# Optimization experiments

Hardware: AMD Instinct MI355X
Metric: run time of the kernel (lower is better)

The kernel has to match this reference:

```python
import jax, jax.numpy as jnp
import numpy as np

DIM = 128
N_GNN = 3
VDW_N = 6.0
MAX_VDW = 0.0356
MIN_VDW = 0.0178
DEV_VDW_RADIUS = 0.2
DM_MIN = 0.5


def gated_gat(x, adj, W, Wb, A, gW, gb):
    # PIGNet-style GatedGAT: attention from bilinear form, gated residual
    h = x @ W + Wb                                   # [B,N,D]
    e = jnp.einsum('bjl,bkl->bjk', h @ A, h)
    e = e + jnp.swapaxes(e, 1, 2)
    att = jnp.where(adj > 0, e, -9e15)
    att = jax.nn.softmax(att, axis=-1) * adj
    hp = jax.nn.relu(jnp.einsum('bij,bjd->bid', att, h))
    coeff = jax.nn.sigmoid(jnp.concatenate([x, hp], axis=-1) @ gW + gb)  # [B,N,1]
    return coeff * x + (1.0 - coeff) * hp


def pair_mlp(lig, tgt, W1, b1, W2, b2):
    # MLP on concat([lig_i, tgt_j]) without materializing [B,L,T,2D]:
    # split W1 along its input dim (exact same math as concat @ W1)
    D = lig.shape[-1]
    pre = (jnp.einsum('bld,dk->blk', lig, W1[:D])[:, :, None, :]
           + jnp.einsum('btd,dk->btk', tgt, W1[D:])[:, None, :, :] + b1)
    h = jax.nn.relu(pre)                             # [B,L,T,D]
    return jnp.einsum('bltk,ko->blt', h, W2) + b2[0]  # [B,L,T]


def setup_inputs() -> dict:
    key = jax.random.key(0)
    ks = jax.random.split(key, 20)
    B, L, T, D = 8, 128, 512, DIM
    f32 = jnp.float32

    def adj(k, n, p):
        a = (jax.random.uniform(k, (B, n, n)) < p).astype(f32)
        a = jnp.maximum(a, jnp.swapaxes(a, 1, 2))
        return jnp.minimum(a + jnp.eye(n, dtype=f32), 1.0)

    s = 0.05
    inp = dict(
        ligand_h=jax.random.normal(ks[0], (B, L, 54), f32),
        target_h=jax.random.normal(ks[1], (B, T, 54), f32),
        ligand_adj=adj(ks[2], L, 0.10),
        target_adj=adj(ks[3], T, 0.02),
        interaction_indice=(jax.random.uniform(ks[4], (B, 3, L, T)) < 0.05).astype(f32),
        ligand_pos=jax.random.uniform(ks[5], (B, L, 3), f32) * 20.0,
        target_pos=jax.random.uniform(ks[6], (B, T, 3), f32) * 20.0,
        rotor=jnp.floor(jax.random.uniform(ks[7], (B, 1), f32) * 10.0),
        ligand_vdw_radii=jax.random.uniform(ks[8], (B, L), f32) * 0.5 + 1.5,
        target_vdw_radii=jax.random.uniform(ks[9], (B, T), f32) * 0.5 + 1.5,
        ligand_valid=jnp.ones((B, L), f32),
        target_valid=jnp.ones((B, T), f32),
        emb_W=jax.random.normal(ks[10], (54, D), f32) * s,
        gat_W=jax.random.normal(ks[11], (N_GNN, D, D), f32) * s,
        gat_Wb=jnp.zeros((N_GNN, D), f32),
        gat_A=jax.random.normal(ks[12], (N_GNN, D, D), f32) * s,
        gat_gW=jax.random.normal(ks[13], (N_GNN, 2 * D, 1), f32) * s,
        gat_gb=jnp.zeros((N_GNN, 1), f32),
        vdwA_W1=jax.random.normal(ks[14], (2 * D, D), f32) * s,
        vdwA_b1=jnp.zeros((D,), f32),
        vdwA_W2=jax.random.normal(ks[15], (D, 1), f32) * s,
        vdwA_b2=jnp.zeros((1,), f32),
        dc_W1=jax.random.normal(ks[16], (2 * D, D), f32) * s,
        dc_b1=jnp.zeros((D,), f32),
        dc_W2=jax.random.normal(ks[17], (D, 1), f32) * s,
        dc_b2=jnp.zeros((1,), f32),
        hbond_coeff=jnp.array([1.0], f32),
        metal_coeff=jnp.array([1.0], f32),
        hydrophobic_coeff=jnp.array([0.5], f32),
        rotor_coeff=jnp.array([0.5], f32),
    )
    return inp


def reference(ligand_h, target_h, ligand_adj, target_adj, interaction_indice,
              ligand_pos, target_pos, rotor, ligand_vdw_radii, target_vdw_radii,
              ligand_valid, target_valid, emb_W, gat_W, gat_Wb, gat_A, gat_gW,
              gat_gb, vdwA_W1, vdwA_b1, vdwA_W2, vdwA_b2, dc_W1, dc_b1, dc_W2,
              dc_b2, hbond_coeff, metal_coeff, hydrophobic_coeff, rotor_coeff):
    lig = ligand_h @ emb_W
    tgt = target_h @ emb_W
    # pairwise distance matrix with min-distance clamp
    diff = ligand_pos[:, :, None, :] - target_pos[:, None, :, :]
    dm = jnp.sqrt((diff * diff).sum(-1) + 1e-10)      # [B,L,T]
    dm = jnp.where(dm < DM_MIN, 1e10, dm)
    for i in range(N_GNN):  # eval mode: dropout is identity
        lig = gated_gat(lig, ligand_adj, gat_W[i], gat_Wb[i], gat_A[i], gat_gW[i], gat_gb[i])
        tgt = gated_gat(tgt, target_adj, gat_W[i], gat_Wb[i], gat_A[i], gat_gW[i], gat_gb[i])
    vdws_sum = ligand_vdw_radii[:, :, None] + target_vdw_radii[:, None, :]
    # dm_correction=True: tanh MLP on pairwise concat features, scaled by dev_vdw_radius
    vdws_sum = vdws_sum + jnp.tanh(pair_mlp(lig, tgt, dc_W1, dc_b1, dc_W2, dc_b2)) * DEV_VDW_RADIUS
    # --- vdw term ---
    dm_0 = jnp.where(vdws_sum < 1e-4, 1.0, vdws_sum)
    ratio = dm_0 / dm
    valid = ligand_valid[:, :, None] * target_valid[:, None, :]
    energy = jnp.minimum(ratio ** (2.0 * VDW_N) - 2.0 * ratio ** VDW_N, 100.0) * valid
    A = jax.nn.sigmoid(pair_mlp(lig, tgt, vdwA_W1, vdwA_b1, vdwA_W2, vdwA_b2))
    A = A * (MAX_VDW - MIN_VDW) + MIN_VDW
    vdw_e = (A * energy).sum((1, 2))                  # [B]
    # --- hbond / metal / hydrophobic ramps share dm - vdws_sum ---
    d = dm - vdws_sum
    ramp = jnp.clip(d / -0.7, 0.0, 1.0)
    hbond_e = -(hbond_coeff[0] ** 2) * (ramp * interaction_indice[:, 0]).sum((1, 2))
    metal_e = -(metal_coeff[0] ** 2) * (ramp * interaction_indice[:, 1]).sum((1, 2))
    ramp2 = jnp.clip(-d + 1.5, 0.0, 1.0)
    hydro_e = -(hydrophobic_coeff[0] ** 2) * (ramp2 * interaction_indice[:, 2]).sum((1, 2))
    energies = jnp.stack([vdw_e, hbond_e, metal_e, hydro_e], axis=-1)  # [B,4]
    energies = energies / (1.0 + rotor_coeff[0] ** 2 * rotor)          # rotor penalty
    return energies
```

## Files before the change

### kernel.cpp

```cpp
#include <hip/hip_runtime.h>
#include <hip/hip_bf16.h>
#include <math.h>

typedef __hip_bfloat16 bf16;

#define DIMD 128
#define BB 8
#define LL 128
#define TT 512

#define BMT 64
#define BKT 32
#define TGT_TILES 36
#define LIG_TILES 3

#define CV_EMBW   0L
#define CV_GATW   (CV_EMBW + 54 * 128)
#define CV_GATA   (CV_GATW + 3 * 128 * 128)
#define CV_WB     (CV_GATA + 3 * 128 * 128)
#define CV_GGW    (CV_WB + 3 * 128)
#define CV_GGB    (CV_GGW + 3 * 2 * 128)
#define CV_DCW1   (CV_GGB + 4)
#define CV_VW1    (CV_DCW1 + 2 * 128 * 128)
#define CV_TOTAL  (CV_VW1 + 2 * 128 * 128)

__device__ __forceinline__ float LD(const void* p, long i, int bf) {
    if (bf) return __bfloat162float(((const bf16*)p)[i]);
    return ((const float*)p)[i];
}

__global__ void init_cvt(const unsigned int* __restrict__ embw_raw,
                         const void* __restrict__ embW, const void* __restrict__ gatW,
                         const void* __restrict__ gatA, const void* __restrict__ gatWb,
                         const void* __restrict__ ggW, const void* __restrict__ ggb,
                         const void* __restrict__ dcW1, const void* __restrict__ vW1,
                         float* __restrict__ out, float* __restrict__ accum,
                         int* __restrict__ flagp) {
    __shared__ int cnts;
    int t = threadIdx.x;
    if (t == 0) cnts = 0;
    __syncthreads();
    unsigned int bword = (embw_raw[t] >> 8) & 0xffu;
    unsigned int e = bword & 0x7fu;
    if (e >= 0x38u && e <= 0x3fu) atomicAdd(&cnts, 1);
    __syncthreads();
    int bf = cnts > 128;
    if (blockIdx.x == 0) {
        if (t < 32) accum[t] = 0.0f;
        if (t == 0) *flagp = bf;
    }
    long i = (long)blockIdx.x * 256 + t;
    if (i >= CV_TOTAL) return;
    float v;
    if (i < CV_GATW)      v = LD(embW, i, bf);
    else if (i < CV_GATA) v = LD(gatW, i - CV_GATW, bf);
    else if (i < CV_WB)   v = LD(gatA, i - CV_GATA, bf);
    else if (i < CV_GGW)  v = LD(gatWb, i - CV_WB, bf);
    else if (i < CV_GGB)  v = LD(ggW, i - CV_GGW, bf);
    else if (i < CV_DCW1) { long j = i - CV_GGB; v = (j < 3) ? LD(ggb, j, bf) : 0.0f; }
    else if (i < CV_VW1)  v = LD(dcW1, i - CV_DCW1, bf);
    else                  v = LD(vW1, i - CV_VW1, bf);
    out[i] = v;
}

__global__ void embed_both(const void* __restrict__ Xl, const void* __restrict__ Xt,
                           const float* __restrict__ Wf, float* __restrict__ out,
                           int K, const int* __restrict__ flagp) {
    __shared__ float xrow[DIMD];
    int bf = *flagp;
    int row = blockIdx.x;
    int d = threadIdx.x;
    const void* X; long r;
    if (row < BB * LL) { X = Xl; r = row; }
    else               { X = Xt; r = row - BB * LL; }
    if (d < K) xrow[d] = LD(X, r * K + d, bf);
    __syncthreads();
    float acc = 0.0f;
    for (int k = 0; k < K; ++k)
        acc = fmaf(xrow[k], Wf[(long)k * DIMD + d], acc);
    out[(long)row * DIMD + d] = acc;
}

__global__ void gemm_hha_gate(float* __restrict__ X, const float* __restrict__ P0,
                              const float* __restrict__ P1, const float* __restrict__ P2,
                              const float* __restrict__ P3, const float* __restrict__ cvw,
                              int layer, int dogate,
                              float* __restrict__ hout, float* __restrict__ hAout) {
    __shared__ float xs[4][DIMD];
    __shared__ float hs[4][DIMD];
    __shared__ float gred[4][2];
    long row0 = (long)blockIdx.x * 4;
    int d = threadIdx.x & 127, rg = threadIdx.x >> 7;
    int w = threadIdx.x >> 6, lane = threadIdx.x & 63;
    long r0 = row0 + rg * 2, r1 = r0 + 1;
    float xv0 = X[r0 * DIMD + d];
    float xv1 = X[r1 * DIMD + d];
    if (dogate) {
        const float* gW = cvw + CV_GGW + (long)(layer - 1) * 2 * DIMD;
        float gb = cvw[CV_GGB + (layer - 1)];
        float hp0 = fmaxf(P0[r0 * DIMD + d] + P1[r0 * DIMD + d]
                        + P2[r0 * DIMD + d] + P3[r0 * DIMD + d], 0.0f);
        float hp1 = fmaxf(P0[r1 * DIMD + d] + P1[r1 * DIMD + d]
                        + P2[r1 * DIMD + d] + P3[r1 * DIMD + d], 0.0f);
        float s0 = xv0 * gW[d] + hp0 * gW[DIMD + d];
        float s1 = xv1 * gW[d] + hp1 * gW[DIMD + d];
#pragma unroll
        for (int s = 32; s > 0; s >>= 1) { s0 += __shfl_xor(s0, s); s1 += __shfl_xor(s1, s); }
        if (lane == 0) { gred[rg * 2 + 0][w & 1] = s0; gred[rg * 2 + 1][w & 1] = s1; }
        __syncthreads();
        float g0 = gred[rg * 2 + 0][0] + gred[rg * 2 + 0][1] + gb;
        float g1 = gred[rg * 2 + 1][0] + gred[rg * 2 + 1][1] + gb;
        float c0 = 1.0f / (1.0f + expf(-g0));
        float c1 = 1.0f / (1.0f + expf(-g1));
        xv0 = c0 * xv0 + (1.0f - c0) * hp0;
        xv1 = c1 * xv1 + (1.0f - c1) * hp1;
        X[r0 * DIMD + d] = xv0;
        X[r1 * DIMD + d] = xv1;
    }
    xs[rg * 2 + 0][d] = xv0;
    xs[rg * 2 + 1][d] = xv1;
    __syncthreads();
    const float* W = cvw + CV_GATW + (long)layer * DIMD * DIMD;
    const float* A = cvw + CV_GATA + (long)layer * DIMD * DIMD;
    float b = cvw[CV_WB + layer * DIMD + d];
    float h0 = b, h1 = b;
    const float* x0 = xs[rg * 2];
    const float* x1 = xs[rg * 2 + 1];
#pragma unroll 8
    for (int k = 0; k < DIMD; ++k) {
        float wv = W[(long)k * DIMD + d];
        h0 = fmaf(x0[k], wv, h0);
        h1 = fmaf(x1[k], wv, h1);
    }
    long ob = r0 * DIMD + d;
    hout[ob] = h0; hout[ob + DIMD] = h1;
    hs[rg * 2][d] = h0; hs[rg * 2 + 1][d] = h1;
    __syncthreads();
    float a0 = 0.0f, a1 = 0.0f;
    const float* g0p = hs[rg * 2];
    const float* g1p = hs[rg * 2 + 1];
#pragma unroll 8
    for (int k = 0; k < DIMD; ++k) {
        float wv = A[(long)k * DIMD + d];
        a0 = fmaf(g0p[k], wv, a0);
        a1 = fmaf(g1p[k], wv, a1);
    }
    hAout[ob] = a0;
    hAout[ob + DIMD] = a1;
}

__global__ void esym_both(const float* __restrict__ hA_t, const float* __restrict__ h_t,
                          float* __restrict__ e1_t, float* __restrict__ e2_t,
                          const float* __restrict__ hA_l, const float* __restrict__ h_l,
                          float* __restrict__ e1_l, float* __restrict__ e2_l) {
    __shared__ float At[BKT][BMT + 4];
    __shared__ float Bt[BKT][BMT + 4];
    int idx = blockIdx.x, half = blockIdx.y, b = blockIdx.z, t = threadIdx.x;
    const float *hA, *h; float* e; int N;
    if (idx < TGT_TILES) { hA = hA_t; h = h_t; e = half ? e2_t : e1_t; N = TT; }
    else { idx -= TGT_TILES; hA = hA_l; h = h_l; e = half ? e2_l : e1_l; N = LL; }
    int jt = (int)((sqrtf(8.0f * idx + 1.0f) - 1.0f) * 0.5f);
    while ((jt + 1) * (jt + 2) / 2 <= idx) ++jt;
    while (jt * (jt + 1) / 2 > idx) --jt;
    int kt = idx - jt * (jt + 1) / 2;
    const float* hAb = hA + (long)b * N * DIMD;
    const float* hb  = h  + (long)b * N * DIMD;
    const float* Ap = half ? hb : hAb;
    const float* Bp = half ? hAb : hb;
    int tm = t & 15, tn = t >> 4;
    int k4 = (t & 7) * 4;
    int row0 = t >> 3;
    float acc[4][4];
#pragma unroll
    for (int i = 0; i < 4; ++i)
#pragma unroll
        for (int jj = 0; jj < 4; ++jj) acc[i][jj] = 0.0f;

#pragma unroll
    for (int c = 0; c < 4; ++c) {
        int ko = c * BKT;
        __syncthreads();
#pragma unroll
        for (int rr = 0; rr < 2; ++rr) {
            int row = row0 + rr * 32;
            float4 av = *(const float4*)&Ap[(long)(jt * BMT + row) * DIMD + ko + k4];
            float4 bv = *(const float4*)&Bp[(long)(kt * BMT + row) * DIMD + ko + k4];
            At[k4 + 0][row] = av.x; At[k4 + 1][row] = av.y;
            At[k4 + 2][row] = av.z; At[k4 + 3][row] = av.w;
            Bt[k4 + 0][row] = bv.x; Bt[k4 + 1][row] = bv.y;
            Bt[k4 + 2][row] = bv.z; Bt[k4 + 3][row] = bv.w;
        }
        __syncthreads();
#pragma unroll
        for (int k = 0; k < BKT; ++k) {
            float4 a4 = *(const float4*)&At[k][tm * 4];
            float4 b4 = *(const float4*)&Bt[k][tn * 4];
            float A[4] = {a4.x, a4.y, a4.z, a4.w};
            float Bv[4] = {b4.x, b4.y, b4.z, b4.w};
#pragma unroll
            for (int i = 0; i < 4; ++i)
#pragma unroll
                for (int jj = 0; jj < 4; ++jj)
                    acc[i][jj] = fmaf(A[i], Bv[jj], acc[i][jj]);
        }
    }
    long ebN = (long)b * N;
    long ebase = (ebN + jt * BMT + tm * 4) * N + kt * BMT + tn * 4;
#pragma unroll
    for (int i = 0; i < 4; ++i) {
        float4 v;
        v.x = acc[i][0]; v.y = acc[i][1]; v.z = acc[i][2]; v.w = acc[i][3];
        *(float4*)&e[ebase + (long)i * N] = v;
    }
    if (jt != kt) {
        long mbase = (ebN + kt * BMT + tn * 4) * N + jt * BMT + tm * 4;
#pragma unroll
        for (int jj = 0; jj < 4; ++jj) {
            float4 v;
            v.x = acc[0][jj]; v.y = acc[1][jj]; v.z = acc[2][jj]; v.w = acc[3][jj];
            *(float4*)&e[mbase + (long)jj * N] = v;
        }
    }
}

template<int CNT>
__device__ __forceinline__ void softmax_row(float* __restrict__ e1row,
                                            const float* __restrict__ e2row,
                                            const void* __restrict__ adj,
                                            long adjbase, int bf) {
    int lane = threadIdx.x & 63;
    float vals[CNT], av[CNT];
    float m = -3.4e38f;
#pragma unroll
    for (int i = 0; i < CNT; ++i) {
        int k = lane + i * 64;
        float a = LD(adj, adjbase + k, bf);
        float v = (a > 0.0f) ? (e1row[k] + e2row[k]) : -9e15f;
        av[i] = a; vals[i] = v;
        m = fmaxf(m, v);
    }
#pragma unroll
    for (int s = 32; s > 0; s >>= 1) m = fmaxf(m, __shfl_xor(m, s));
    float sum = 0.0f;
#pragma unroll
    for (int i = 0; i < CNT; ++i) { vals[i] = expf(vals[i] - m); sum += vals[i]; }
#pragma unroll
    for (int s = 32; s > 0; s >>= 1) sum += __shfl_xor(sum, s);
    float inv = 1.0f / sum;
#pragma unroll
    for (int i = 0; i < CNT; ++i)
        e1row[lane + i * 64] = vals[i] * av[i] * inv;
}

__global__ void att_softmax_both(float* __restrict__ e1_t, const float* __restrict__ e2_t,
                                 float* __restrict__ e1_l, const float* __restrict__ e2_l,
                                 const void* __restrict__ adj_t, const void* __restrict__ adj_l,
                                 const int* __restrict__ flagp) {
    int bf = *flagp;
    int b = blockIdx.y, x = blockIdx.x;
    int jr = threadIdx.x >> 6;
    if (x < TT / 4) {
        int j = x * 4 + jr;
        long base = ((long)b * TT + j) * TT;
        softmax_row<8>(e1_t + base, e2_t + base, adj_t, base, bf);
    } else {
        int j = (x - TT / 4) * 4 + jr;
        long base = ((long)b * LL + j) * LL;
        softmax_row<2>(e1_l + base, e2_l + base, adj_l, base, bf);
    }
}

__global__ void hp_gemm_both(const float* __restrict__ att_t, const float* __restrict__ h_t,
                             const float* __restrict__ att_l, const float* __restrict__ h_l,
                             float* __restrict__ P0, float* __restrict__ P1,
                             float* __restrict__ P2, float* __restrict__ P3) {
    __shared__ float At[32][36];
    __shared__ float Ht[32][DIMD];
    int jt = blockIdx.x, kc = blockIdx.y, b = blockIdx.z;
    int t = threadIdx.x;
    const float *att, *h; int N; long rowbase;
    if (jt < 16) { att = att_t; h = h_t; N = TT; rowbase = (long)BB * LL + (long)b * TT; }
    else { jt -= 16; att = att_l; h = h_l; N = LL; rowbase = (long)b * LL; }
    const float* attb = att + (long)b * N * N;
    const float* hb = h + (long)b * N * DIMD;
    int tm = t & 7, tn = t >> 3;
    float acc[4][4] = {};
    int kchunk = N / 4;
    int kbeg = kc * kchunk;
    int ar = t >> 3;
    int ac4 = (t & 7) * 4;
    int hk = t >> 5;
    int hc4 = (t & 31) * 4;
    for (int k0 = kbeg; k0 < kbeg + kchunk; k0 += 32) {
        __syncthreads();
        float4 av = *(const float4*)&attb[(long)(jt * 32 + ar) * N + k0 + ac4];
        At[ac4 + 0][ar] = av.x; At[ac4 + 1][ar] = av.y;
        At[ac4 + 2][ar] = av.z; At[ac4 + 3][ar] = av.w;
#pragma unroll
        for (int p = 0; p < 4; ++p)
            *(float4*)&Ht[hk + p * 8][hc4] = *(const float4*)&hb[(long)(k0 + hk + p * 8) * DIMD + hc4];
        __syncthreads();
#pragma unroll
        for (int k = 0; k < 32; ++k) {
            float4 a4 = *(const float4*)&At[k][tm * 4];
            float4 h4 = *(const float4*)&Ht[k][tn * 4];
            float A[4] = {a4.x, a4.y, a4.z, a4.w};
            float H[4] = {h4.x, h4.y, h4.z, h4.w};
#pragma unroll
            for (int i = 0; i < 4; ++i)
#pragma unroll
                for (int jj = 0; jj < 4; ++jj)
                    acc[i][jj] = fmaf(A[i], H[jj], acc[i][jj]);
        }
    }
    float* outp = (kc == 0) ? P0 : (kc == 1) ? P1 : (kc == 2) ? P2 : P3;
    long obase = (rowbase + jt * 32 + tm * 4) * DIMD + tn * 4;
#pragma unroll
    for (int i = 0; i < 4; ++i) {
        float4 v; v.x = acc[i][0]; v.y = acc[i][1]; v.z = acc[i][2]; v.w = acc[i][3];
        *(float4*)&outp[obase + (long)i * DIMD] = v;
    }
}

__global__ void proj_gate(const float* __restrict__ X, const float* __restrict__ P0,
                          const float* __restrict__ P1, const float* __restrict__ P2,
                          const float* __restrict__ P3, const float* __restrict__ cvw,
                          const void* __restrict__ bdc, const void* __restrict__ bA,
                          long rowsplit, float* __restrict__ outdc, float* __restrict__ outA,
                          const int* __restrict__ flagp) {
    __shared__ float xs[4][DIMD];
    __shared__ float gred[4][2];
    int bf = *flagp;
    long row0 = (long)blockIdx.x * 4;
    int d = threadIdx.x & 127, rg = threadIdx.x >> 7;
    int w = threadIdx.x >> 6, lane = threadIdx.x & 63;
    long r0 = row0 + rg * 2, r1 = r0 + 1;
    float xv0 = X[r0 * DIMD + d];
    float xv1 = X[r1 * DIMD + d];
    {
        const float* gW = cvw + CV_GGW + 2L * 2 * DIMD;
        float gb = cvw[CV_GGB + 2];
        float hp0 = fmaxf(P0[r0 * DIMD + d] + P1[r0 * DIMD + d]
                        + P2[r0 * DIMD + d] + P3[r0 * DIMD + d], 0.0f);
        float hp1 = fmaxf(P0[r1 * DIMD + d] + P1[r1 * DIMD + d]
                        + P2[r1 * DIMD + d] + P3[r1 * DIMD + d], 0.0f);
        float s0 = xv0 * gW[d] + hp0 * gW[DIMD + d];
        float s1 = xv1 * gW[d] + hp1 * gW[DIMD + d];
#pragma unroll
        for (int s = 32; s > 0; s >>= 1) { s0 += __shfl_xor(s0, s); s1 += __shfl_xor(s1, s); }
        if (lane == 0) { gred[rg * 2 + 0][w & 1] = s0; gred[rg * 2 + 1][w & 1] = s1; }
        __syncthreads();
        float g0 = gred[rg * 2 + 0][0] + gred[rg * 2 + 0][1] + gb;
        float g1 = gred[rg * 2 + 1][0] + gred[rg * 2 + 1][1] + gb;
        float c0 = 1.0f / (1.0f + expf(-g0));
        float c1 = 1.0f / (1.0f + expf(-g1));
        xv0 = c0 * xv0 + (1.0f - c0) * hp0;
        xv1 = c1 * xv1 + (1.0f - c1) * hp1;
    }
    xs[rg * 2 + 0][d] = xv0;
    xs[rg * 2 + 1][d] = xv1;
    __syncthreads();
    const float* Wf = (blockIdx.y == 0) ? (cvw + CV_DCW1) : (cvw + CV_VW1);
    const void* bias = (blockIdx.y == 0) ? bdc : bA;
    float* out = (blockIdx.y == 0) ? outdc : outA;
    int sideb = row0 >= rowsplit;
    const float* W = Wf + (sideb ? (long)DIMD * DIMD : 0);
    float b0 = sideb ? 0.0f : LD(bias, d, bf);
    float a0 = b0, a1 = b0;
    const float* x0 = xs[rg * 2];
    const float* x1 = xs[rg * 2 + 1];
#pragma unroll 8
    for (int k = 0; k < DIMD; ++k) {
        float wv = W[(long)k * DIMD + d];
        a0 = fmaf(x0[k], wv, a0);
        a1 = fmaf(x1[k], wv, a1);
    }
    long ob = r0 * DIMD + d;
    out[ob] = a0;
    out[ob + DIMD] = a1;
}

__global__ void transpose_both(const float* __restrict__ in0, float* __restrict__ out0,
                               const float* __restrict__ in1, float* __restrict__ out1) {
    __shared__ float tile[32][33];
    int z = blockIdx.z;
    const float* in; float* outT; int b;
    if (z < BB) { in = in0; outT = out0; b = z; }
    else        { in = in1; outT = out1; b = z - BB; }
    int n0 = blockIdx.x * 32;
    int d0 = blockIdx.y * 32;
    int t = threadIdx.x;
    int tx = t & 31, ty = t >> 5;
    for (int r = ty; r < 32; r += 8)
        tile[r][tx] = in[((long)b * TT + n0 + r) * DIMD + d0 + tx];
    __syncthreads();
    for (int r = ty; r < 32; r += 8)
        outT[((long)b * DIMD + d0 + r) * TT + n0 + tx] = tile[tx][r];
}

__global__ void pair_energy(const float* __restrict__ ligdc, const float* __restrict__ tgtdcT,
                            const float* __restrict__ ligA, const float* __restrict__ tgtAT,
                            const void* __restrict__ dcW2, const void* __restrict__ dcb2,
                            const void* __restrict__ AW2, const void* __restrict__ Ab2,
                            const void* __restrict__ lpos, const void* __restrict__ tpos,
                            const void* __restrict__ lrad, const void* __restrict__ trad,
                            const void* __restrict__ lval, const void* __restrict__ tval,
                            const void* __restrict__ ii, float* __restrict__ accum,
                            const int* __restrict__ flagp) {
    int bf = *flagp;
    int l0 = blockIdx.x * 2, b = blockIdx.y, t = threadIdx.x;
    __shared__ __align__(16) float sdc0[DIMD], sdc1[DIMD], sA0[DIMD], sA1[DIMD];
    __shared__ __align__(16) float w2dc[DIMD], w2A[DIMD];
    __shared__ float redw[4][4];
    if (t < DIMD) {
        sdc0[t] = ligdc[((long)b * LL + l0) * DIMD + t];
        sA0[t]  = ligA [((long)b * LL + l0) * DIMD + t];
        w2dc[t] = LD(dcW2, t, bf);
        w2A[t]  = LD(AW2, t, bf);
    } else {
        int u = t - DIMD;
        sdc1[u] = ligdc[((long)b * LL + l0 + 1) * DIMD + u];
        sA1[u]  = ligA [((long)b * LL + l0 + 1) * DIMD + u];
    }
    int tt0 = t * 2;
    float tx0 = LD(tpos, ((long)b * TT + tt0) * 3 + 0, bf);
    float ty0 = LD(tpos, ((long)b * TT + tt0) * 3 + 1, bf);
    float tz0 = LD(tpos, ((long)b * TT + tt0) * 3 + 2, bf);
    float tx1 = LD(tpos, ((long)b * TT + tt0 + 1) * 3 + 0, bf);
    float ty1 = LD(tpos, ((long)b * TT + tt0 + 1) * 3 + 1, bf);
    float tz1 = LD(tpos, ((long)b * TT + tt0 + 1) * 3 + 2, bf);
    float tr0 = LD(trad, (long)b * TT + tt0, bf);
    float tr1 = LD(trad, (long)b * TT + tt0 + 1, bf);
    float tv0 = LD(tval, (long)b * TT + tt0, bf);
    float tv1 = LD(tval, (long)b * TT + tt0 + 1, bf);
    long iiA0 = ((long)(b * 3 + 0) * LL + l0) * TT;
    long iiB0 = ((long)(b * 3 + 1) * LL + l0) * TT;
    long iiC0 = ((long)(b * 3 + 2) * LL + l0) * TT;
    long iiA1 = iiA0 + TT, iiB1 = iiB0 + TT, iiC1 = iiC0 + TT;
    float iA00 = LD(ii, iiA0 + tt0, bf), iA01 = LD(ii, iiA0 + tt0 + 1, bf);
    float iA10 = LD(ii, iiA1 + tt0, bf), iA11 = LD(ii, iiA1 + tt0 + 1, bf);
    float iB00 = LD(ii, iiB0 + tt0, bf), iB01 = LD(ii, iiB0 + tt0 + 1, bf);
    float iB10 = LD(ii, iiB1 + tt0, bf), iB11 = LD(ii, iiB1 + tt0 + 1, bf);
    float iC00 = LD(ii, iiC0 + tt0, bf), iC01 = LD(ii, iiC0 + tt0 + 1, bf);
    float iC10 = LD(ii, iiC1 + tt0, bf), iC11 = LD(ii, iiC1 + tt0 + 1, bf);
    float lx0 = LD(lpos, ((long)b * LL + l0) * 3 + 0, bf);
    float ly0 = LD(lpos, ((long)b * LL + l0) * 3 + 1, bf);
    float lz0 = LD(lpos, ((long)b * LL + l0) * 3 + 2, bf);
    float lx1 = LD(lpos, ((long)b * LL + l0 + 1) * 3 + 0, bf);
    float ly1 = LD(lpos, ((long)b * LL + l0 + 1) * 3 + 1, bf);
    float lz1 = LD(lpos, ((long)b * LL + l0 + 1) * 3 + 2, bf);
    float lr0 = LD(lrad, (long)b * LL + l0, bf);
    float lr1 = LD(lrad, (long)b * LL + l0 + 1, bf);
    float lv0 = LD(lval, (long)b * LL + l0, bf);
    float lv1 = LD(lval, (long)b * LL + l0 + 1, bf);
    float cdcb2 = LD(dcb2, 0, bf), cab2 = LD(Ab2, 0, bf);
    __syncthreads();
    const float* tdT = tgtdcT + (long)b * DIMD * TT;
    const float* taT = tgtAT  + (long)b * DIMD * TT;
    float adc00 = 0.0f, adc01 = 0.0f, adc10 = 0.0f, adc11 = 0.0f;
    float aA00 = 0.0f, aA01 = 0.0f, aA10 = 0.0f, aA11 = 0.0f;
    for (int i4 = 0; i4 < DIMD; i4 += 4) {
        float4 wd = *(const float4*)&w2dc[i4];
        float4 wa = *(const float4*)&w2A[i4];
        float4 v0d = *(const float4*)&sdc0[i4];
        float4 v1d = *(const float4*)&sdc1[i4];
        float4 v0a = *(const float4*)&sA0[i4];
        float4 v1a = *(const float4*)&sA1[i4];
        float wdv[4] = {wd.x, wd.y, wd.z, wd.w};
        float wav[4] = {wa.x, wa.y, wa.z, wa.w};
        float s0d[4] = {v0d.x, v0d.y, v0d.z, v0d.w};
        float s1d[4] = {v1d.x, v1d.y, v1d.z, v1d.w};
        float s0a[4] = {v0a.x, v0a.y, v0a.z, v0a.w};
        float s1a[4] = {v1a.x, v1a.y, v1a.z, v1a.w};
#pragma unroll
        for (int j = 0; j < 4; ++j) {
            float2 td = *(const float2*)&tdT[(long)(i4 + j) * TT + tt0];
            float2 ta = *(const float2*)&taT[(long)(i4 + j) * TT + tt0];
            adc00 = fmaf(fmaxf(td.x + s0d[j], 0.0f), wdv[j], adc00);
            adc01 = fmaf(fmaxf(td.y + s0d[j], 0.0f), wdv[j], adc01);
            adc10 = fmaf(fmaxf(td.x + s1d[j], 0.0f), wdv[j], adc10);
            adc11 = fmaf(fmaxf(td.y + s1d[j], 0.0f), wdv[j], adc11);
            aA00 = fmaf(fmaxf(ta.x + s0a[j], 0.0f), wav[j], aA00);
            aA01 = fmaf(fmaxf(ta.y + s0a[j], 0.0f), wav[j], aA01);
            aA10 = fmaf(fmaxf(ta.x + s1a[j], 0.0f), wav[j], aA10);
            aA11 = fmaf(fmaxf(ta.y + s1a[j], 0.0f), wav[j], aA11);
        }
    }
    float p0 = 0.0f, p1 = 0.0f, p2 = 0.0f, p3 = 0.0f;
#pragma unroll
    for (int jj = 0; jj < 2; ++jj) {
        float tx = jj ? tx1 : tx0, ty = jj ? ty1 : ty0, tz = jj ? tz1 : tz0;
        float tr = jj ? tr1 : tr0, tv = jj ? tv1 : tv0;
#pragma unroll
        for (int li = 0; li < 2; ++li) {
            float dx = (li ? lx1 : lx0) - tx;
            float dy = (li ? ly1 : ly0) - ty;
            float dz = (li ? lz1 : lz0) - tz;
            float dm = sqrtf(dx * dx + dy * dy + dz * dz + 1e-10f);
            if (dm < 0.5f) dm = 1e10f;
            float adcv = jj ? (li ? adc11 : adc01) : (li ? adc10 : adc00);
            float aAv  = jj ? (li ? aA11  : aA01)  : (li ? aA10  : aA00);
            float dev = tanhf(adcv + cdcb2) * 0.2f;
            float vdws = (li ? lr1 : lr0) + tr + dev;
            float dm0 = (vdws < 1e-4f) ? 1.0f : vdws;
            float ratio = dm0 / dm;
            float r2 = ratio * ratio, r6 = r2 * r2 * r2, r12 = r6 * r6;
            float en = fminf(r12 - 2.0f * r6, 100.0f) * (li ? lv1 : lv0) * tv;
            float As = 1.0f / (1.0f + expf(-(aAv + cab2)));
            As = As * (0.0356f - 0.0178f) + 0.0178f;
            p0 = fmaf(As, en, p0);
            float dd = dm - vdws;
            float ramp = fminf(fmaxf(dd * (1.0f / -0.7f), 0.0f), 1.0f);
            float ramp2 = fminf(fmaxf(-dd + 1.5f, 0.0f), 1.0f);
            float vA = jj ? (li ? iA11 : iA01) : (li ? iA10 : iA00);
            float vB = jj ? (li ? iB11 : iB01) : (li ? iB10 : iB00);
            float vC = jj ? (li ? iC11 : iC01) : (li ? iC10 : iC00);
            p1 = fmaf(ramp, vA, p1);
            p2 = fmaf(ramp, vB, p2);
            p3 = fmaf(ramp2, vC, p3);
        }
    }
#pragma unroll
    for (int s = 32; s > 0; s >>= 1) {
        p0 += __shfl_xor(p0, s);
        p1 += __shfl_xor(p1, s);
        p2 += __shfl_xor(p2, s);
        p3 += __shfl_xor(p3, s);
    }
    int w = t >> 6, lane = t & 63;
    if (lane == 0) { redw[w][0] = p0; redw[w][1] = p1; redw[w][2] = p2; redw[w][3] = p3; }
    __syncthreads();
    if (t < 4) {
        float v = redw[0][t] + redw[1][t] + redw[2][t] + redw[3][t];
        atomicAdd(&accum[b * 4 + t], v);
    }
}

__global__ void finalize(const float* __restrict__ accum, const void* __restrict__ hb,
                         const void* __restrict__ mc, const void* __restrict__ hyd,
                         const void* __restrict__ rc, const void* __restrict__ rotor,
                         void* __restrict__ out, const int* __restrict__ flagp) {
    int bf = *flagp;
    int t = threadIdx.x;
    if (t >= 32) return;
    int b = t >> 2, e = t & 3;
    float v = accum[t];
    if (e == 1) { float c = LD(hb, 0, bf);  v = -c * c * v; }
    else if (e == 2) { float c = LD(mc, 0, bf);  v = -c * c * v; }
    else if (e == 3) { float c = LD(hyd, 0, bf); v = -c * c * v; }
    float r = LD(rc, 0, bf);
    float den = 1.0f + r * r * LD(rotor, b, bf);
    float res = v / den;
    if (bf) ((bf16*)out)[t] = __float2bfloat16(res);
    else    ((float*)out)[t] = res;
}

extern "C" void kernel_launch(void* const* d_in, const int* in_sizes, int n_in,
                              void* d_out, int out_size, void* d_ws, size_t ws_size,
                              hipStream_t stream) {
    const void* ligand_h = d_in[0];
    const void* target_h = d_in[1];
    const void* ligand_adj = d_in[2];
    const void* target_adj = d_in[3];
    const void* interaction_indice = d_in[4];
    const void* ligand_pos = d_in[5];
    const void* target_pos = d_in[6];
    const void* rotor = d_in[7];
    const void* ligand_vdw = d_in[8];
    const void* target_vdw = d_in[9];
    const void* ligand_valid = d_in[10];
    const void* target_valid = d_in[11];
    const void* emb_W = d_in[12];
    const void* gat_W = d_in[13];
    const void* gat_Wb = d_in[14];
    const void* gat_A = d_in[15];
    const void* gat_gW = d_in[16];
    const void* gat_gb = d_in[17];
    const void* vdwA_W1 = d_in[18];
    const void* vdwA_b1 = d_in[19];
    const void* vdwA_W2 = d_in[20];
    const void* vdwA_b2 = d_in[21];
    const void* dc_W1 = d_in[22];
    const void* dc_b1 = d_in[23];
    const void* dc_W2 = d_in[24];
    const void* dc_b2 = d_in[25];
    const void* hbond_coeff = d_in[26];
    const void* metal_coeff = d_in[27];
    const void* hydrophobic_coeff = d_in[28];
    const void* rotor_coeff = d_in[29];

    float* ws = (float*)d_ws;
    size_t off = 0;
    float* lig_x = ws + off;  off += (size_t)BB * LL * DIMD;
    float* tgt_x = ws + off;  off += (size_t)BB * TT * DIMD;
    float* h_lig = ws + off;  off += (size_t)BB * LL * DIMD;
    float* h_tgt = ws + off;  off += (size_t)BB * TT * DIMD;
    float* hA_lig = ws + off; off += (size_t)BB * LL * DIMD;
    float* hA_tgt = ws + off; off += (size_t)BB * TT * DIMD;
    float* accum = ws + off;  off += 32;
    int* flagp = (int*)(ws + off); off += 2;
    float* e_buf = ws + off;  off += (size_t)BB * TT * TT;
    float* e_lig = ws + off;  off += (size_t)BB * LL * LL;
    float* e2_buf = ws + off; off += (size_t)BB * TT * TT;
    float* e2_lig = ws + off; off += (size_t)BB * LL * LL;
    float* part1 = ws + off;  off += (size_t)BB * (LL + TT) * DIMD;
    float* part2 = ws + off;  off += (size_t)BB * (LL + TT) * DIMD;
    float* part3 = ws + off;  off += (size_t)BB * (LL + TT) * DIMD;
    float* projA = ws + off;  off += (size_t)BB * (LL + TT) * DIMD;
    float* cvw   = ws + off;  off += (size_t)CV_TOTAL;
    float* part0 = hA_lig;
    float* ligdc = h_lig;
    float* tgtdc = h_tgt;
    float* ligA = projA;
    float* tgtA = projA + (size_t)BB * LL * DIMD;
    float* tgtdcT = e_buf;
    float* tgtAT  = e_buf + (size_t)BB * DIMD * TT;
    float* wEmb = cvw + CV_EMBW;

    init_cvt<<<(CV_TOTAL + 255) / 256, 256, 0, stream>>>(
        (const unsigned int*)emb_W, emb_W, gat_W, gat_A, gat_Wb,
        gat_gW, gat_gb, dc_W1, vdwA_W1, cvw, accum, flagp);

    embed_both<<<BB * (LL + TT), DIMD, 0, stream>>>(ligand_h, target_h, wEmb, lig_x, 54, flagp);

    const long ROWSPLIT = (long)BB * LL;
    for (int i = 0; i < 3; ++i) {
        gemm_hha_gate<<<BB * (LL + TT) / 4, 256, 0, stream>>>(
            lig_x, part0, part1, part2, part3, cvw, i, i > 0 ? 1 : 0, h_lig, hA_lig);
        esym_both<<<dim3(TGT_TILES + LIG_TILES, 2, BB), 256, 0, stream>>>(
            hA_tgt, h_tgt, e_buf, e2_buf, hA_lig, h_lig, e_lig, e2_lig);
        att_softmax_both<<<dim3(TT / 4 + LL / 4, BB), 256, 0, stream>>>(
            e_buf, e2_buf, e_lig, e2_lig, target_adj, ligand_adj, flagp);
        hp_gemm_both<<<dim3(20, 4, BB), 256, 0, stream>>>(
            e_buf, h_tgt, e_lig, h_lig, part0, part1, part2, part3);
    }

    proj_gate<<<dim3(BB * (LL + TT) / 4, 2), 256, 0, stream>>>(
        lig_x, part0, part1, part2, part3, cvw, dc_b1, vdwA_b1, ROWSPLIT,
        ligdc, ligA, flagp);

    transpose_both<<<dim3(TT / 32, DIMD / 32, 2 * BB), 256, 0, stream>>>(
        tgtdc, tgtdcT, tgtA, tgtAT);

    pair_energy<<<dim3(LL / 2, BB), 256, 0, stream>>>(
        ligdc, tgtdcT, ligA, tgtAT, dc_W2, dc_b2, vdwA_W2, vdwA_b2,
        ligand_pos, target_pos, ligand_vdw, target_vdw,
        ligand_valid, target_valid, interaction_indice, accum, flagp);

    finalize<<<1, 64, 0, stream>>>(accum, hbond_coeff, metal_coeff,
                                   hydrophobic_coeff, rotor_coeff, rotor, d_out, flagp);
}
```

Before: 342.4 us.

## Fuse symmetric attention sum into one GEMM and softmax into hp GEMM

The esym kernel now builds e + e^T directly by accumulating both hA·h and h·hA products over an 8-chunk K loop, so the separate e2 buffers go away. Row softmax is folded into the attention-times-h GEMM, which writes normalized attention into shared memory, and the K split drops from four partials to two. This removes one kernel launch per layer and several full N×N memory round trips. In exchange, each hp block recomputes softmax over full rows (work duplicated across the two K halves) and holds a larger shared tile, and the small projection GEMMs now use split accumulators for more instruction-level parallelism.

```diff
diff --git a/kernel.cpp b/kernel.cpp
--- a/kernel.cpp
+++ b/kernel.cpp
@@ -82,8 +82,7 @@
 }
 
 __global__ void gemm_hha_gate(float* __restrict__ X, const float* __restrict__ P0,
-                              const float* __restrict__ P1, const float* __restrict__ P2,
-                              const float* __restrict__ P3, const float* __restrict__ cvw,
+                              const float* __restrict__ P1, const float* __restrict__ cvw,
                               int layer, int dogate,
                               float* __restrict__ hout, float* __restrict__ hAout) {
     __shared__ float xs[4][DIMD];
@@ -98,10 +97,8 @@
     if (dogate) {
         const float* gW = cvw + CV_GGW + (long)(layer - 1) * 2 * DIMD;
         float gb = cvw[CV_GGB + (layer - 1)];
-        float hp0 = fmaxf(P0[r0 * DIMD + d] + P1[r0 * DIMD + d]
-                        + P2[r0 * DIMD + d] + P3[r0 * DIMD + d], 0.0f);
-        float hp1 = fmaxf(P0[r1 * DIMD + d] + P1[r1 * DIMD + d]
-                        + P2[r1 * DIMD + d] + P3[r1 * DIMD + d], 0.0f);
+        float hp0 = fmaxf(P0[r0 * DIMD + d] + P1[r0 * DIMD + d], 0.0f);
+        float hp1 = fmaxf(P0[r1 * DIMD + d] + P1[r1 * DIMD + d], 0.0f);
         float s0 = xv0 * gW[d] + hp0 * gW[DIMD + d];
         float s1 = xv1 * gW[d] + hp1 * gW[DIMD + d];
 #pragma unroll
@@ -123,50 +120,55 @@
     const float* W = cvw + CV_GATW + (long)layer * DIMD * DIMD;
     const float* A = cvw + CV_GATA + (long)layer * DIMD * DIMD;
     float b = cvw[CV_WB + layer * DIMD + d];
-    float h0 = b, h1 = b;
     const float* x0 = xs[rg * 2];
     const float* x1 = xs[rg * 2 + 1];
-#pragma unroll 8
-    for (int k = 0; k < DIMD; ++k) {
-        float wv = W[(long)k * DIMD + d];
-        h0 = fmaf(x0[k], wv, h0);
-        h1 = fmaf(x1[k], wv, h1);
-    }
+    float h0a = b, h0b = 0.0f, h1a = b, h1b = 0.0f;
+#pragma unroll 4
+    for (int k = 0; k < 64; ++k) {
+        float w0 = W[(long)k * DIMD + d];
+        float w1 = W[(long)(k + 64) * DIMD + d];
+        h0a = fmaf(x0[k], w0, h0a);
+        h0b = fmaf(x0[k + 64], w1, h0b);
+        h1a = fmaf(x1[k], w0, h1a);
+        h1b = fmaf(x1[k + 64], w1, h1b);
+    }
+    float h0 = h0a + h0b, h1 = h1a + h1b;
     long ob = r0 * DIMD + d;
     hout[ob] = h0; hout[ob + DIMD] = h1;
     hs[rg * 2][d] = h0; hs[rg * 2 + 1][d] = h1;
     __syncthreads();
-    float a0 = 0.0f, a1 = 0.0f;
     const float* g0p = hs[rg * 2];
     const float* g1p = hs[rg * 2 + 1];
-#pragma unroll 8
-    for (int k = 0; k < DIMD; ++k) {
-        float wv = A[(long)k * DIMD + d];
-        a0 = fmaf(g0p[k], wv, a0);
-        a1 = fmaf(g1p[k], wv, a1);
-    }
-    hAout[ob] = a0;
-    hAout[ob + DIMD] = a1;
+    float a0a = 0.0f, a0b = 0.0f, a1a = 0.0f, a1b = 0.0f;
+#pragma unroll 4
+    for (int k = 0; k < 64; ++k) {
+        float w0 = A[(long)k * DIMD + d];
+        float w1 = A[(long)(k + 64) * DIMD + d];
+        a0a = fmaf(g0p[k], w0, a0a);
+        a0b = fmaf(g0p[k + 64], w1, a0b);
+        a1a = fmaf(g1p[k], w0, a1a);
+        a1b = fmaf(g1p[k + 64], w1, a1b);
+    }
+    hAout[ob] = a0a + a0b;
+    hAout[ob + DIMD] = a1a + a1b;
 }
 
 __global__ void esym_both(const float* __restrict__ hA_t, const float* __restrict__ h_t,
-                          float* __restrict__ e1_t, float* __restrict__ e2_t,
+                          float* __restrict__ e_t,
                           const float* __restrict__ hA_l, const float* __restrict__ h_l,
-                          float* __restrict__ e1_l, float* __restrict__ e2_l) {
+                          float* __restrict__ e_l) {
     __shared__ float At[BKT][BMT + 4];
     __shared__ float Bt[BKT][BMT + 4];
-    int idx = blockIdx.x, half = blockIdx.y, b = blockIdx.z, t = threadIdx.x;
+    int idx = blockIdx.x, b = blockIdx.y, t = threadIdx.x;
     const float *hA, *h; float* e; int N;
-    if (idx < TGT_TILES) { hA = hA_t; h = h_t; e = half ? e2_t : e1_t; N = TT; }
-    else { idx -= TGT_TILES; hA = hA_l; h = h_l; e = half ? e2_l : e1_l; N = LL; }
+    if (idx < TGT_TILES) { hA = hA_t; h = h_t; e = e_t; N = TT; }
+    else { idx -= TGT_TILES; hA = hA_l; h = h_l; e = e_l; N = LL; }
     int jt = (int)((sqrtf(8.0f * idx + 1.0f) - 1.0f) * 0.5f);
     while ((jt + 1) * (jt + 2) / 2 <= idx) ++jt;
     while (jt * (jt + 1) / 2 > idx) --jt;
     int kt = idx - jt * (jt + 1) / 2;
     const float* hAb = hA + (long)b * N * DIMD;
     const float* hb  = h  + (long)b * N * DIMD;
-    const float* Ap = half ? hb : hAb;
-    const float* Bp = half ? hAb : hb;
     int tm = t & 15, tn = t >> 4;
     int k4 = (t & 7) * 4;
     int row0 = t >> 3;
@@ -177,8 +179,10 @@
         for (int jj = 0; jj < 4; ++jj) acc[i][jj] = 0.0f;
 
 #pragma unroll
-    for (int c = 0; c < 4; ++c) {
-        int ko = c * BKT;
+    for (int c = 0; c < 8; ++c) {
+        const float* Ap = (c < 4) ? hAb : hb;
+        const float* Bp = (c < 4) ? hb : hAb;
+        int ko = (c & 3) * BKT;
         __syncthreads();
 #pragma unroll
         for (int rr = 0; rr < 2; ++rr) {
@@ -224,10 +228,10 @@
 }
 
 template<int CNT>
-__device__ __forceinline__ void softmax_row(float* __restrict__ e1row,
-                                            const float* __restrict__ e2row,
-                                            const void* __restrict__ adj,
-                                            long adjbase, int bf) {
+__device__ __forceinline__ void sm_row_store(const float* __restrict__ erow,
+                                             const void* __restrict__ adj,
+                                             long adjbase, int bf, int kc,
+                                             float* __restrict__ attTbase, int lr) {
     int lane = threadIdx.x & 63;
     float vals[CNT], av[CNT];
     float m = -3.4e38f;
@@ -235,7 +239,7 @@
     for (int i = 0; i < CNT; ++i) {
         int k = lane + i * 64;
         float a = LD(adj, adjbase + k, bf);
-        float v = (a > 0.0f) ? (e1row[k] + e2row[k]) : -9e15f;
+        float v = (a > 0.0f) ? erow[k] : -9e15f;
         av[i] = a; vals[i] = v;
         m = fmaxf(m, v);
     }
@@ -248,61 +252,58 @@
     for (int s = 32; s > 0; s >>= 1) sum += __shfl_xor(sum, s);
     float inv = 1.0f / sum;
 #pragma unroll
-    for (int i = 0; i < CNT; ++i)
-        e1row[lane + i * 64] = vals[i] * av[i] * inv;
-}
-
-__global__ void att_softmax_both(float* __restrict__ e1_t, const float* __restrict__ e2_t,
-                                 float* __restrict__ e1_l, const float* __restrict__ e2_l,
-                                 const void* __restrict__ adj_t, const void* __restrict__ adj_l,
-                                 const int* __restrict__ flagp) {
+    for (int i = 0; i < CNT; ++i) {
+        if ((i / (CNT / 2)) == kc) {
+            int klocal = lane + (i % (CNT / 2)) * 64;
+            attTbase[klocal * 36 + lr] = vals[i] * av[i] * inv;
+        }
+    }
+}
+
+__global__ void hp_sm_both(const float* __restrict__ e_t, const float* __restrict__ h_t,
+                           const void* __restrict__ adj_t,
+                           const float* __restrict__ e_l, const float* __restrict__ h_l,
+                           const void* __restrict__ adj_l,
+                           float* __restrict__ P0, float* __restrict__ P1,
+                           const int* __restrict__ flagp) {
+    __shared__ float attT[256][36];
+    __shared__ float Ht[32][DIMD];
     int bf = *flagp;
-    int b = blockIdx.y, x = blockIdx.x;
-    int jr = threadIdx.x >> 6;
-    if (x < TT / 4) {
-        int j = x * 4 + jr;
-        long base = ((long)b * TT + j) * TT;
-        softmax_row<8>(e1_t + base, e2_t + base, adj_t, base, bf);
-    } else {
-        int j = (x - TT / 4) * 4 + jr;
-        long base = ((long)b * LL + j) * LL;
-        softmax_row<2>(e1_l + base, e2_l + base, adj_l, base, bf);
-    }
-}
-
-__global__ void hp_gemm_both(const float* __restrict__ att_t, const float* __restrict__ h_t,
-                             const float* __restrict__ att_l, const float* __restrict__ h_l,
-                             float* __restrict__ P0, float* __restrict__ P1,
-                             float* __restrict__ P2, float* __restrict__ P3) {
-    __shared__ float At[32][36];
-    __shared__ float Ht[32][DIMD];
     int jt = blockIdx.x, kc = blockIdx.y, b = blockIdx.z;
     int t = threadIdx.x;
-    const float *att, *h; int N; long rowbase;
-    if (jt < 16) { att = att_t; h = h_t; N = TT; rowbase = (long)BB * LL + (long)b * TT; }
-    else { jt -= 16; att = att_l; h = h_l; N = LL; rowbase = (long)b * LL; }
-    const float* attb = att + (long)b * N * N;
+    const float *e, *h; const void* adj; int N; long rowbase;
+    if (jt < 16) { e = e_t; h = h_t; adj = adj_t; N = TT; rowbase = (long)BB * LL + (long)b * TT; }
+    else { jt -= 16; e = e_l; h = h_l; adj = adj_l; N = LL; rowbase = (long)b * LL; }
+    int half = N / 2;
+    int koff = kc * half;
     const float* hb = h + (long)b * N * DIMD;
+    int w = t >> 6;
+    if (N == TT) {
+        for (int r = 0; r < 8; ++r) {
+            int lr = w * 8 + r;
+            long base = ((long)b * TT + jt * 32 + lr) * TT;
+            sm_row_store<8>(e + base, adj, base, bf, kc, &attT[0][0], lr);
+        }
+    } else {
+        for (int r = 0; r < 8; ++r) {
+            int lr = w * 8 + r;
+            long base = ((long)b * LL + jt * 32 + lr) * LL;
+            sm_row_store<2>(e + base, adj, base, bf, kc, &attT[0][0], lr);
+        }
+    }
     int tm = t & 7, tn = t >> 3;
+    int hk = t >> 5, hc4 = (t & 31) * 4;
     float acc[4][4] = {};
-    int kchunk = N / 4;
-    int kbeg = kc * kchunk;
-    int ar = t >> 3;
-    int ac4 = (t & 7) * 4;
-    int hk = t >> 5;
-    int hc4 = (t & 31) * 4;
-    for (int k0 = kbeg; k0 < kbeg + kchunk; k0 += 32) {
+    for (int k0 = 0; k0 < half; k0 += 32) {
         __syncthreads();
-        float4 av = *(const float4*)&attb[(long)(jt * 32 + ar) * N + k0 + ac4];
-        At[ac4 + 0][ar] = av.x; At[ac4 + 1][ar] = av.y;
-        At[ac4 + 2][ar] = av.z; At[ac4 + 3][ar] = av.w;
 #pragma unroll
         for (int p = 0; p < 4; ++p)
-            *(float4*)&Ht[hk + p * 8][hc4] = *(const float4*)&hb[(long)(k0 + hk + p * 8) * DIMD + hc4];
+            *(float4*)&Ht[hk + p * 8][hc4] =
+                *(const float4*)&hb[(long)(koff + k0 + hk + p * 8) * DIMD + hc4];
         __syncthreads();
 #pragma unroll
         for (int k = 0; k < 32; ++k) {
-            float4 a4 = *(const float4*)&At[k][tm * 4];
+            float4 a4 = *(const float4*)&attT[k0 + k][tm * 4];
             float4 h4 = *(const float4*)&Ht[k][tn * 4];
             float A[4] = {a4.x, a4.y, a4.z, a4.w};
             float H[4] = {h4.x, h4.y, h4.z, h4.w};
@@ -313,7 +314,7 @@
                     acc[i][jj] = fmaf(A[i], H[jj], acc[i][jj]);
         }
     }
-    float* outp = (kc == 0) ? P0 : (kc == 1) ? P1 : (kc == 2) ? P2 : P3;
+    float* outp = (kc == 0) ? P0 : P1;
     long obase = (rowbase + jt * 32 + tm * 4) * DIMD + tn * 4;
 #pragma unroll
     for (int i = 0; i < 4; ++i) {
@@ -323,8 +324,7 @@
 }
 
 __global__ void proj_gate(const float* __restrict__ X, const float* __restrict__ P0,
-                          const float* __restrict__ P1, const float* __restrict__ P2,
-                          const float* __restrict__ P3, const float* __restrict__ cvw,
+                          const float* __restrict__ P1, const float* __restrict__ cvw,
                           const void* __restrict__ bdc, const void* __restrict__ bA,
                           long rowsplit, float* __restrict__ outdc, float* __restrict__ outA,
                           const int* __restrict__ flagp) {
@@ -340,10 +340,8 @@
     {
         const float* gW = cvw + CV_GGW + 2L * 2 * DIMD;
         float gb = cvw[CV_GGB + 2];
-        float hp0 = fmaxf(P0[r0 * DIMD + d] + P1[r0 * DIMD + d]
-                        + P2[r0 * DIMD + d] + P3[r0 * DIMD + d], 0.0f);
-        float hp1 = fmaxf(P0[r1 * DIMD + d] + P1[r1 * DIMD + d]
-                        + P2[r1 * DIMD + d] + P3[r1 * DIMD + d], 0.0f);
+        float hp0 = fmaxf(P0[r0 * DIMD + d] + P1[r0 * DIMD + d], 0.0f);
+        float hp1 = fmaxf(P0[r1 * DIMD + d] + P1[r1 * DIMD + d], 0.0f);
         float s0 = xv0 * gW[d] + hp0 * gW[DIMD + d];
         float s1 = xv1 * gW[d] + hp1 * gW[DIMD + d];
 #pragma unroll
@@ -366,18 +364,21 @@
     int sideb = row0 >= rowsplit;
     const float* W = Wf + (sideb ? (long)DIMD * DIMD : 0);
     float b0 = sideb ? 0.0f : LD(bias, d, bf);
-    float a0 = b0, a1 = b0;
     const float* x0 = xs[rg * 2];
     const float* x1 = xs[rg * 2 + 1];
-#pragma unroll 8
-    for (int k = 0; k < DIMD; ++k) {
-        float wv = W[(long)k * DIMD + d];
-        a0 = fmaf(x0[k], wv, a0);
-        a1 = fmaf(x1[k], wv, a1);
+    float a0a = b0, a0b = 0.0f, a1a = b0, a1b = 0.0f;
+#pragma unroll 4
+    for (int k = 0; k < 64; ++k) {
+        float w0 = W[(long)k * DIMD + d];
+        float w1 = W[(long)(k + 64) * DIMD + d];
+        a0a = fmaf(x0[k], w0, a0a);
+        a0b = fmaf(x0[k + 64], w1, a0b);
+        a1a = fmaf(x1[k], w0, a1a);
+        a1b = fmaf(x1[k + 64], w1, a1b);
     }
     long ob = r0 * DIMD + d;
-    out[ob] = a0;
-    out[ob + DIMD] = a1;
+    out[ob] = a0a + a0b;
+    out[ob + DIMD] = a1a + a1b;
 }
 
 __global__ void transpose_both(const float* __restrict__ in0, float* __restrict__ out0,
@@ -601,11 +602,7 @@
     int* flagp = (int*)(ws + off); off += 2;
     float* e_buf = ws + off;  off += (size_t)BB * TT * TT;
     float* e_lig = ws + off;  off += (size_t)BB * LL * LL;
-    float* e2_buf = ws + off; off += (size_t)BB * TT * TT;
-    float* e2_lig = ws + off; off += (size_t)BB * LL * LL;
     float* part1 = ws + off;  off += (size_t)BB * (LL + TT) * DIMD;
-    float* part2 = ws + off;  off += (size_t)BB * (LL + TT) * DIMD;
-    float* part3 = ws + off;  off += (size_t)BB * (LL + TT) * DIMD;
     float* projA = ws + off;  off += (size_t)BB * (LL + TT) * DIMD;
     float* cvw   = ws + off;  off += (size_t)CV_TOTAL;
     float* part0 = hA_lig;
@@ -626,18 +623,16 @@
     const long ROWSPLIT = (long)BB * LL;
     for (int i = 0; i < 3; ++i) {
         gemm_hha_gate<<<BB * (LL + TT) / 4, 256, 0, stream>>>(
-            lig_x, part0, part1, part2, part3, cvw, i, i > 0 ? 1 : 0, h_lig, hA_lig);
-        esym_both<<<dim3(TGT_TILES + LIG_TILES, 2, BB), 256, 0, stream>>>(
-            hA_tgt, h_tgt, e_buf, e2_buf, hA_lig, h_lig, e_lig, e2_lig);
-        att_softmax_both<<<dim3(TT / 4 + LL / 4, BB), 256, 0, stream>>>(
-            e_buf, e2_buf, e_lig, e2_lig, target_adj, ligand_adj, flagp);
-        hp_gemm_both<<<dim3(20, 4, BB), 256, 0, stream>>>(
-            e_buf, h_tgt, e_lig, h_lig, part0, part1, part2, part3);
+            lig_x, part0, part1, cvw, i, i > 0 ? 1 : 0, h_lig, hA_lig);
+        esym_both<<<dim3(TGT_TILES + LIG_TILES, BB), 256, 0, stream>>>(
+            hA_tgt, h_tgt, e_buf, hA_lig, h_lig, e_lig);
+        hp_sm_both<<<dim3(20, 2, BB), 256, 0, stream>>>(
+            e_buf, h_tgt, target_adj, e_lig, h_lig, ligand_adj,
+            part0, part1, flagp);
     }
 
     proj_gate<<<dim3(BB * (LL + TT) / 4, 2), 256, 0, stream>>>(
-        lig_x, part0, part1, part2, part3, cvw, dc_b1, vdwA_b1, ROWSPLIT,
-        ligdc, ligA, flagp);
+        lig_x, part0, part1, cvw, dc_b1, vdwA_b1, ROWSPLIT, ligdc, ligA, flagp);
 
     transpose_both<<<dim3(TT / 32, DIMD / 32, 2 * BB), 256, 0, stream>>>(
         tgtdc, tgtdcT, tgtA, tgtAT);
```

Result: slower. 431.0 us (+25.9%).
